# Kernel optimization log

Hardware: AMD Instinct MI355X
Metric: run time of the kernel (lower is better)

Reference implementation:

```python
import jax, jax.numpy as jnp
import numpy as np
import math

B_GRAPHS = 256
L_NODES = 64
N_NODES = B_GRAPHS * L_NODES
N_EDGES = N_NODES * 4
HEADS = 8
D_INNER = 512
N_DAGS = 1
DIAMETER = 64


def setup_inputs() -> dict:
    key = jax.random.key(0)
    ks = jax.random.split(key, 8)
    x = jax.random.normal(ks[0], (N_NODES, D_INNER), jnp.float32)
    B = jax.random.normal(ks[1], (N_NODES, D_INNER), jnp.float32)
    C = jax.random.normal(ks[2], (N_NODES, D_INNER), jnp.float32)
    dt = jax.random.normal(ks[3], (N_NODES, N_DAGS * HEADS * 2), jnp.float32)
    dt_edge = jax.random.normal(ks[4], (N_EDGES, N_DAGS * HEADS), jnp.float32)
    # DAG edges: within each graph, src_local < dst_local (gap 1..7) -> strictly upper triangular
    u = jax.random.randint(ks[5], (N_EDGES,), 0, L_NODES - 1)
    gap = jax.random.randint(ks[6], (N_EDGES,), 1, 8)
    v = jnp.minimum(u + gap, L_NODES - 1)
    graph = jnp.arange(N_EDGES) // (N_EDGES // B_GRAPHS)
    edge_index = jnp.stack([graph * L_NODES + u, graph * L_NODES + v]).astype(jnp.int32)
    data_batch = (jnp.arange(N_NODES) // L_NODES).astype(jnp.int32)
    dag_masks = jnp.ones((N_DAGS, N_EDGES), jnp.float32)
    # dt_bias init as in module __init__ (inverse softplus of dt in [1e-3, 1e-1])
    rng = np.random.default_rng(0)
    dtv = np.exp(rng.uniform(size=(HEADS,)) * (math.log(0.1) - math.log(0.001)) + math.log(0.001))
    dtv = np.clip(dtv, 1e-4, None)
    dt_bias = jnp.asarray(dtv + np.log(-np.expm1(-dtv)), jnp.float32)
    D = jnp.ones((HEADS,), jnp.float32)
    return dict(x=x, B=B, C=C, dt=dt, dt_edge=dt_edge, dt_bias=dt_bias, D=D,
                dag_masks=dag_masks, edge_index=edge_index, data_batch=data_batch,
                diameter=DIAMETER)


def _repeated_squaring_inverse(A, diam):
    # (I - A)^{-1} = prod_k (I + A^{2^k}) for nilpotent A; O(log diam) matmuls
    j = 2 ** int(math.ceil(math.log2(diam)))
    I = jnp.eye(A.shape[-1], dtype=A.dtype)
    last = A
    M = I + A
    for _ in range(2, int(math.log2(j)) + 1):
        last = last @ last
        M = M @ (I + last)
    return M


def reference(x, B, C, dt, dt_edge, dt_bias, D, dag_masks, edge_index, data_batch, diameter):
    N, din = x.shape
    g, E = dag_masks.shape
    n = dt_bias.shape[0]
    b = int(data_batch[-1]) + 1
    l = N // b  # equal-size graphs -> dense batching is a reshape, mask all-True
    h = din // n
    src, dst = edge_index[0], edge_index[1]

    # dt_node: (N, g*n*c) -> (c, g, n, N); softplus(dt + bias)
    c = dt.shape[1] // (g * n)
    dtn = dt.reshape(N, g, n, c).transpose(3, 1, 2, 0)
    dtn = jax.nn.softplus(dtn + dt_bias[None, None, :, None])
    dte = dt_edge.reshape(E, g, n).transpose(1, 2, 0)  # (g,n,E)
    dte = jax.nn.softplus(dte + dt_bias[None, :, None])

    dt_s, dt_t = dtn[0], dtn[1]
    dt_sum = (dt_s[:, :, src] + dt_t[:, :, dst] + dte) / np.sqrt(3.0)  # (g,n,E)
    dt_exp = jnp.exp(-dt_sum)
    msk = dag_masks[:, None, :]
    dt_sum = dt_sum * msk
    dt_exp = dt_exp * msk

    # dense adjacency with per-edge attrs; note 'b l1 l2 (g n) -> b g n l2 l1' transpose
    b_e = src // l
    sl = src % l
    dl = dst % l
    attr = dt_exp.transpose(2, 0, 1).reshape(E, g * n)
    adj = jnp.zeros((b, l, l, g * n), x.dtype).at[b_e, sl, dl].add(attr)
    A = adj.reshape(b, l, l, g, n).transpose(0, 3, 4, 2, 1)  # (b,g,n,l,l)

    # normalize_mat: sqrt outer product of in-degree counts, clamped at 1
    ec = jnp.zeros((g, N), x.dtype).at[:, dst].add(dag_masks)
    ec_dense = ec.T.reshape(b, l, g)
    outer = jnp.sqrt(jnp.einsum('blg,btg->bglt', ec_dense, ec_dense))
    outer = jnp.where(outer < 1.0, 1.0, outer)
    A = A / outer[:, :, None]

    dnorm = jnp.zeros((g, n, N), x.dtype).at[:, :, dst].add(dt_sum)
    dnorm = dnorm.transpose(2, 0, 1).reshape(b, l, g, n).transpose(0, 2, 3, 1)  # (b,g,n,l)

    A2 = A.reshape(b, g * n, l, l).astype(jnp.float32)
    L = _repeated_squaring_inverse(A2, int(diameter))
    L = L.reshape(b, g, n, l, l) * dnorm[..., None]

    x4 = x.reshape(b, l, n, h).transpose(0, 2, 1, 3)  # (b,n,l,h)
    B3 = B.reshape(b, l, -1)
    C3 = C.reshape(b, l, -1)
    # y = einsum(C,L,B,x) with B/C broadcast over (g,n): fold C.B^T into L
    CB = jnp.einsum('bld,btd->blt', C3, B3)
    M = L * CB[:, None, None]
    y = jnp.einsum('bgnlt,bnth->bgnlh', M, x4)
    y = y + x4[:, None] * D[None, None, :, None, None]
    y = y.transpose(0, 3, 1, 2, 4).reshape(N, g, n * h)  # b g n l h -> (N, g, n*h)
    y = y.sum(axis=1) / np.sqrt(g)
    return y
```

## Files before the change

### kernel.cpp

```cpp
#include <hip/hip_runtime.h>
#include <math.h>

#define NGRAPH 256
#define LNODE  64
#define HEADS  8
#define DIN    512
#define EPG    256
#define NEDGE  65536

__device__ __forceinline__ float softplusf(float v) {
    return (v > 20.f) ? v : log1pf(expf(v));
}
__device__ __forceinline__ unsigned short f2bf(float f) {
    union { float f; unsigned u; } c; c.f = f;
    unsigned r = c.u + 0x7fffu + ((c.u >> 16) & 1u);
    return (unsigned short)(r >> 16);
}
__device__ __forceinline__ float bf2f(unsigned short h) {
    union { float f; unsigned u; } c; c.u = ((unsigned)h) << 16;
    return c.f;
}

__global__ __launch_bounds__(256) void cb_kernel(const float* __restrict__ Bm,
                                                 const float* __restrict__ Cm,
                                                 float* __restrict__ CBp,
                                                 int dper, int tposed) {
    int b = blockIdx.x;
    int slice = blockIdx.y;
    __shared__ float Cs[64 * 68];
    __shared__ float Bs[64 * 68];
    int tid = threadIdx.x;
    int ti = tid >> 4, tj = tid & 15;
    float acc[4][4] = {};
    const float* Cg = Cm + (size_t)b * 64 * DIN;
    const float* Bg = Bm + (size_t)b * 64 * DIN;
    int d_lo = slice * dper;
    for (int d0 = d_lo; d0 < d_lo + dper; d0 += 64) {
        __syncthreads();
        #pragma unroll
        for (int k = 0; k < 4; ++k) {
            int f = k * 256 + tid;
            int row = f >> 4;
            int c4 = (f & 15) << 2;
            *(float4*)(Cs + row * 68 + c4) = *(const float4*)(Cg + row * DIN + d0 + c4);
            *(float4*)(Bs + row * 68 + c4) = *(const float4*)(Bg + row * DIN + d0 + c4);
        }
        __syncthreads();
        for (int d = 0; d < 64; d += 4) {
            float4 cr[4], br[4];
            #pragma unroll
            for (int r = 0; r < 4; ++r) cr[r] = *(const float4*)(Cs + (4 * ti + r) * 68 + d);
            #pragma unroll
            for (int c = 0; c < 4; ++c) br[c] = *(const float4*)(Bs + (4 * tj + c) * 68 + d);
            #pragma unroll
            for (int r = 0; r < 4; ++r)
                #pragma unroll
                for (int c = 0; c < 4; ++c)
                    acc[r][c] += cr[r].x * br[c].x + cr[r].y * br[c].y +
                                 cr[r].z * br[c].z + cr[r].w * br[c].w;
        }
    }
    float* outp = CBp + ((size_t)slice * NGRAPH + b) * 4096;
    if (!tposed) {
        #pragma unroll
        for (int r = 0; r < 4; ++r)
            *(float4*)(outp + (4 * ti + r) * 64 + 4 * tj) =
                make_float4(acc[r][0], acc[r][1], acc[r][2], acc[r][3]);
    } else {
        #pragma unroll
        for (int r = 0; r < 4; ++r)
            #pragma unroll
            for (int c = 0; c < 4; ++c)
                outp[(4 * tj + c) * 64 + (4 * ti + r)] = acc[r][c];
    }
}

__global__ __launch_bounds__(256) void prep_kernel(const float* __restrict__ dt,
                                                   const float* __restrict__ dt_edge,
                                                   const float* __restrict__ dt_bias,
                                                   const float* __restrict__ Dp,
                                                   const float* __restrict__ dag_masks,
                                                   const int* __restrict__ edge_index,
                                                   const float* __restrict__ CBp,
                                                   unsigned short* __restrict__ Wtg,
                                                   int nslice) {
    int b = blockIdx.x;
    int hq = blockIdx.y;
    int tid = threadIdx.x;
    int w = tid >> 6;
    int lane = tid & 63;
    int head = hq * 4 + w;

    __shared__ float CBsh[4096];
    __shared__ unsigned short Wt[4][4096];
    __shared__ float Ab[4][512];
    __shared__ float dnsh[4][64];
    __shared__ float dts[4][64];
    __shared__ float dtt[4][64];
    __shared__ float ecsh[4][64];

    for (int s4 = tid; s4 < 1024; s4 += 256) {
        float4 v = make_float4(0.f, 0.f, 0.f, 0.f);
        for (int s = 0; s < nslice; ++s) {
            float4 p = *(const float4*)(CBp + ((size_t)s * NGRAPH + b) * 4096 + s4 * 4);
            v.x += p.x; v.y += p.y; v.z += p.z; v.w += p.w;
        }
        *(float4*)(CBsh + s4 * 4) = v;
    }
    #pragma unroll
    for (int k = 0; k < 8; ++k) Ab[w][k * 64 + lane] = 0.f;
    dnsh[w][lane] = 0.f;
    ecsh[w][lane] = 0.f;
    float bias = dt_bias[head];
    {
        int node = b * 64 + lane;
        dts[w][lane] = softplusf(dt[node * 16 + head * 2 + 0] + bias);
        dtt[w][lane] = softplusf(dt[node * 16 + head * 2 + 1] + bias);
    }
    __syncthreads();

    #pragma unroll
    for (int k = 0; k < 4; ++k) {
        int e = b * EPG + k * 64 + lane;
        int sl = edge_index[e] & 63;
        int dl = edge_index[NEDGE + e] & 63;
        float m = dag_masks[e];
        float de = softplusf(dt_edge[e * HEADS + head] + bias);
        float dsum = (dts[w][sl] + dtt[w][dl] + de) * 0.57735026918962576451f;
        float dexp = expf(-dsum);
        atomicAdd(&Ab[w][dl * 8 + (dl - sl)], dexp * m);
        atomicAdd(&dnsh[w][dl], dsum * m);
        atomicAdd(&ecsh[w][dl], m);
    }

    {
        float eci = ecsh[w][lane];
        #pragma unroll
        for (int d = 1; d < 8; ++d) {
            int s_ = lane - d;
            if (s_ >= 0) {
                float den = sqrtf(eci * ecsh[w][s_]);
                if (den < 1.f) den = 1.f;
                Ab[w][lane * 8 + d] = Ab[w][lane * 8 + d] / den;
            }
        }
    }

    {
        int j = lane;
        float Dh = Dp[head];
        float mwin[7] = {0.f, 0.f, 0.f, 0.f, 0.f, 0.f, 0.f};
        for (int i8 = 0; i8 < 8; ++i8) {
            unsigned pk[4];
            #pragma unroll
            for (int u = 0; u < 8; ++u) {
                int i = i8 * 8 + u;
                float mi = (j == i) ? 1.f : 0.f;
                #pragma unroll
                for (int s = 0; s < 7; ++s) mi += Ab[w][i * 8 + s + 1] * mwin[s];
                float wv = mi * CBsh[i * 64 + j] * dnsh[w][i];
                if (j == i) wv += Dh;
                #pragma unroll
                for (int s = 6; s > 0; --s) mwin[s] = mwin[s - 1];
                mwin[0] = mi;
                unsigned short hb = f2bf(wv);
                if (u & 1) pk[u >> 1] |= ((unsigned)hb) << 16;
                else       pk[u >> 1] = (unsigned)hb;
            }
            int cblk = i8 ^ (j & 7);
            *(uint4*)(&Wt[w][j * 64 + cblk * 8]) = make_uint4(pk[0], pk[1], pk[2], pk[3]);
        }
    }
    __syncthreads();

    {
        size_t ghbase = ((size_t)b * HEADS + head) * 4096;
        int r_off = lane >> 3;
        int ibk = lane & 7;
        #pragma unroll
        for (int r0 = 0; r0 < 64; r0 += 8) {
            int r = r0 + r_off;
            int cblk = ibk ^ (r & 7);
            uint4 v = *(const uint4*)(&Wt[w][r * 64 + cblk * 8]);
            *(uint4*)(Wtg + ghbase + (size_t)r * 64 + ibk * 8) = v;
        }
    }
}

__global__ __launch_bounds__(256) void gemm_kernel(const float* __restrict__ x,
                                                   const unsigned short* __restrict__ Wtg,
                                                   float* __restrict__ out) {
    int b = blockIdx.x;
    int head = blockIdx.y;
    __shared__ unsigned short Wt[64 * 72];
    __shared__ float Xs[64 * 64];
    int tid = threadIdx.x;

    const uint4* wg = (const uint4*)(Wtg + ((size_t)b * HEADS + head) * 4096);
    #pragma unroll
    for (int q = 0; q < 2; ++q) {
        int s = q * 256 + tid;
        int row = s >> 3;
        int c8 = (s & 7) * 8;
        *(uint4*)(&Wt[row * 72 + c8]) = wg[s];
    }
    const float* xg0 = x + (size_t)b * 64 * DIN + head * 64;
    #pragma unroll
    for (int k = 0; k < 4; ++k) {
        int s = k * 256 + tid;
        int row = s >> 4;
        int c4 = (s & 15) << 2;
        *(float4*)(Xs + row * 64 + c4) = *(const float4*)(xg0 + (size_t)row * DIN + c4);
    }
    __syncthreads();

    int ti = tid >> 4, tj = tid & 15;
    float acc[4][4] = {};
    #pragma unroll 4
    for (int t = 0; t < 64; ++t) {
        uint2 wp = *(const uint2*)(&Wt[t * 72 + 4 * ti]);
        float w0 = bf2f((unsigned short)(wp.x & 0xffffu));
        float w1 = bf2f((unsigned short)(wp.x >> 16));
        float w2 = bf2f((unsigned short)(wp.y & 0xffffu));
        float w3 = bf2f((unsigned short)(wp.y >> 16));
        float4 xv = *(const float4*)(Xs + t * 64 + 4 * tj);
        acc[0][0] += w0 * xv.x; acc[0][1] += w0 * xv.y; acc[0][2] += w0 * xv.z; acc[0][3] += w0 * xv.w;
        acc[1][0] += w1 * xv.x; acc[1][1] += w1 * xv.y; acc[1][2] += w1 * xv.z; acc[1][3] += w1 * xv.w;
        acc[2][0] += w2 * xv.x; acc[2][1] += w2 * xv.y; acc[2][2] += w2 * xv.z; acc[2][3] += w2 * xv.w;
        acc[3][0] += w3 * xv.x; acc[3][1] += w3 * xv.y; acc[3][2] += w3 * xv.z; acc[3][3] += w3 * xv.w;
    }
    #pragma unroll
    for (int r = 0; r < 4; ++r) {
        int i = 4 * ti + r;
        *(float4*)(out + ((size_t)(b * 64 + i)) * DIN + head * 64 + 4 * tj) =
            make_float4(acc[r][0], acc[r][1], acc[r][2], acc[r][3]);
    }
}

__global__ __launch_bounds__(256, 4) void fused_kernel(const float* __restrict__ x,
                                                       const float* __restrict__ dt,
                                                       const float* __restrict__ dt_edge,
                                                       const float* __restrict__ dt_bias,
                                                       const float* __restrict__ Dp,
                                                       const float* __restrict__ dag_masks,
                                                       const int* __restrict__ edge_index,
                                                       const float* __restrict__ CBt,
                                                       float* __restrict__ out,
                                                       int nslice) {
    int b = blockIdx.x;
    int head = blockIdx.y;
    __shared__ float Ab[64 * 8];
    __shared__ float Mt[64 * 68];
    __shared__ float Xs[64 * 64];
    __shared__ float dnsh[64];
    __shared__ float ecsh[64];
    __shared__ float dts[64];
    __shared__ float dtt[64];
    int tid = threadIdx.x;

    int t4 = tid >> 2;
    int ib = (tid & 3) << 4;
    float4 cbsum[4];
    #pragma unroll
    for (int g = 0; g < 4; ++g) cbsum[g] = make_float4(0.f, 0.f, 0.f, 0.f);
    for (int s = 0; s < nslice; ++s) {
        const float* p = CBt + ((size_t)s * NGRAPH + b) * 4096 + t4 * 64 + ib;
        #pragma unroll
        for (int g = 0; g < 4; ++g) {
            float4 v = *(const float4*)(p + 4 * g);
            cbsum[g].x += v.x; cbsum[g].y += v.y; cbsum[g].z += v.z; cbsum[g].w += v.w;
        }
    }
    const float* xg0 = x + ((size_t)b * 64) * DIN + head * 64;
    #pragma unroll
    for (int k = 0; k < 4; ++k) {
        int s = k * 256 + tid;
        int row = s >> 4;
        int c4 = (s & 15) << 2;
        *(float4*)(Xs + row * 64 + c4) = *(const float4*)(xg0 + (size_t)row * DIN + c4);
    }
    for (int k = tid; k < 512; k += 256) Ab[k] = 0.f;
    float bias = dt_bias[head];
    if (tid < 64) {
        dnsh[tid] = 0.f;
        ecsh[tid] = 0.f;
        int node = b * 64 + tid;
        dts[tid] = softplusf(dt[node * 16 + head * 2 + 0] + bias);
        dtt[tid] = softplusf(dt[node * 16 + head * 2 + 1] + bias);
    }
    __syncthreads();
    {
        int e = b * EPG + tid;
        int sl = edge_index[e] & 63;
        int dl = edge_index[NEDGE + e] & 63;
        float m = dag_masks[e];
        float de = softplusf(dt_edge[e * HEADS + head] + bias);
        float dsum = (dts[sl] + dtt[dl] + de) * 0.57735026918962576451f;
        float dexp = expf(-dsum);
        atomicAdd(&Ab[dl * 8 + (dl - sl)], dexp * m);
        atomicAdd(&dnsh[dl], dsum * m);
        atomicAdd(&ecsh[dl], m);
    }
    __syncthreads();
    for (int k = tid; k < 512; k += 256) {
        int i = k >> 3, d = k & 7;
        int src = i - d;
        if (d >= 1 && src >= 0) {
            float den = sqrtf(ecsh[i] * ecsh[src]);
            if (den < 1.f) den = 1.f;
            Ab[k] = Ab[k] / den;
        }
    }
    __syncthreads();
    if (tid < 64) {
        int j = tid;
        float mwin[7] = {0.f, 0.f, 0.f, 0.f, 0.f, 0.f, 0.f};
        for (int i = 0; i < 64; ++i) {
            float mi = (j == i) ? 1.f : 0.f;
            #pragma unroll
            for (int s = 0; s < 7; ++s) mi += Ab[i * 8 + s + 1] * mwin[s];
            Mt[j * 65 + i] = mi;
            #pragma unroll
            for (int s = 6; s > 0; --s) mwin[s] = mwin[s - 1];
            mwin[0] = mi;
        }
    }
    __syncthreads();
    {
        float wv[16];
        #pragma unroll
        for (int g = 0; g < 4; ++g) {
            float4 dn4 = *(const float4*)(dnsh + ib + 4 * g);
            wv[4 * g + 0] = Mt[t4 * 65 + ib + 4 * g + 0] * cbsum[g].x * dn4.x;
            wv[4 * g + 1] = Mt[t4 * 65 + ib + 4 * g + 1] * cbsum[g].y * dn4.y;
            wv[4 * g + 2] = Mt[t4 * 65 + ib + 4 * g + 2] * cbsum[g].z * dn4.z;
            wv[4 * g + 3] = Mt[t4 * 65 + ib + 4 * g + 3] * cbsum[g].w * dn4.w;
        }
        __syncthreads();
        #pragma unroll
        for (int g = 0; g < 4; ++g)
            *(float4*)(Mt + t4 * 68 + ib + 4 * g) =
                make_float4(wv[4 * g + 0], wv[4 * g + 1], wv[4 * g + 2], wv[4 * g + 3]);
    }
    __syncthreads();
    int ti = tid >> 4, tj = tid & 15;
    float acc[4][4] = {};
    #pragma unroll 4
    for (int t = 0; t < 64; ++t) {
        float4 w4 = *(const float4*)(Mt + t * 68 + 4 * ti);
        float4 xv = *(const float4*)(Xs + t * 64 + 4 * tj);
        acc[0][0] += w4.x * xv.x; acc[0][1] += w4.x * xv.y; acc[0][2] += w4.x * xv.z; acc[0][3] += w4.x * xv.w;
        acc[1][0] += w4.y * xv.x; acc[1][1] += w4.y * xv.y; acc[1][2] += w4.y * xv.z; acc[1][3] += w4.y * xv.w;
        acc[2][0] += w4.z * xv.x; acc[2][1] += w4.z * xv.y; acc[2][2] += w4.z * xv.z; acc[2][3] += w4.z * xv.w;
        acc[3][0] += w4.w * xv.x; acc[3][1] += w4.w * xv.y; acc[3][2] += w4.w * xv.z; acc[3][3] += w4.w * xv.w;
    }
    float Dh = Dp[head];
    #pragma unroll
    for (int r = 0; r < 4; ++r) {
        int i = 4 * ti + r;
        float4 xres = *(const float4*)(Xs + i * 64 + 4 * tj);
        float4 v;
        v.x = acc[r][0] + xres.x * Dh;
        v.y = acc[r][1] + xres.y * Dh;
        v.z = acc[r][2] + xres.z * Dh;
        v.w = acc[r][3] + xres.w * Dh;
        *(float4*)(out + ((size_t)(b * 64 + i)) * DIN + head * 64 + 4 * tj) = v;
    }
}

extern "C" void kernel_launch(void* const* d_in, const int* in_sizes, int n_in,
                              void* d_out, int out_size, void* d_ws, size_t ws_size,
                              hipStream_t stream) {
    const float* x        = (const float*)d_in[0];
    const float* Bm       = (const float*)d_in[1];
    const float* Cm       = (const float*)d_in[2];
    const float* dt       = (const float*)d_in[3];
    const float* dt_edge  = (const float*)d_in[4];
    const float* dt_bias  = (const float*)d_in[5];
    const float* Dp       = (const float*)d_in[6];
    const float* dag_mask = (const float*)d_in[7];
    const int*   edge_idx = (const int*)d_in[8];
    float* out = (float*)d_out;

    const size_t CBSLICE = (size_t)NGRAPH * 4096 * 4;
    const size_t WBYTES  = (size_t)NGRAPH * HEADS * 4096 * 2;

    int nslice;
    bool fused;
    if (ws_size >= WBYTES + 4 * CBSLICE)      { fused = false; nslice = 4; }
    else if (ws_size >= WBYTES + 2 * CBSLICE) { fused = false; nslice = 2; }
    else if (ws_size >= WBYTES + 1 * CBSLICE) { fused = false; nslice = 1; }
    else { fused = true; nslice = (ws_size >= 4 * CBSLICE) ? 4 : 1; }

    float* CBp = (float*)d_ws;
    int dper = DIN / nslice;

    if (!fused) {
        unsigned short* Wtg = (unsigned short*)((char*)d_ws + nslice * CBSLICE);
        cb_kernel<<<dim3(NGRAPH, nslice), 256, 0, stream>>>(Bm, Cm, CBp, dper, 0);
        prep_kernel<<<dim3(NGRAPH, 2), 256, 0, stream>>>(dt, dt_edge, dt_bias, Dp,
                                                         dag_mask, edge_idx, CBp, Wtg, nslice);
        gemm_kernel<<<dim3(NGRAPH, HEADS), 256, 0, stream>>>(x, Wtg, out);
    } else {
        cb_kernel<<<dim3(NGRAPH, nslice), 256, 0, stream>>>(Bm, Cm, CBp, dper, 1);
        fused_kernel<<<dim3(NGRAPH, HEADS), 256, 0, stream>>>(x, dt, dt_edge, dt_bias, Dp,
                                                              dag_mask, edge_idx, CBp, out, nslice);
    }
}
```

Baseline: 193.3 us.

## Fuse prep and GEMM into one kernel using bf16 MFMA

Result: no change. 192.7 us (-0.3%).

```diff
diff --git a/kernel.cpp b/kernel.cpp
--- a/kernel.cpp
+++ b/kernel.cpp
@@ -7,6 +7,9 @@
 #define DIN    512
 #define EPG    256
 #define NEDGE  65536
+
+typedef short bf16x8 __attribute__((ext_vector_type(8)));
+typedef float f32x4 __attribute__((ext_vector_type(4)));
 
 __device__ __forceinline__ float softplusf(float v) {
     return (v > 20.f) ? v : log1pf(expf(v));
@@ -75,29 +78,29 @@
     }
 }
 
-__global__ __launch_bounds__(256) void prep_kernel(const float* __restrict__ dt,
-                                                   const float* __restrict__ dt_edge,
-                                                   const float* __restrict__ dt_bias,
-                                                   const float* __restrict__ Dp,
-                                                   const float* __restrict__ dag_masks,
-                                                   const int* __restrict__ edge_index,
-                                                   const float* __restrict__ CBp,
-                                                   unsigned short* __restrict__ Wtg,
-                                                   int nslice) {
+__global__ __launch_bounds__(256, 4) void fused2_kernel(const float* __restrict__ x,
+                                                        const float* __restrict__ dt,
+                                                        const float* __restrict__ dt_edge,
+                                                        const float* __restrict__ dt_bias,
+                                                        const float* __restrict__ Dp,
+                                                        const float* __restrict__ dag_masks,
+                                                        const int* __restrict__ edge_index,
+                                                        const float* __restrict__ CBp,
+                                                        float* __restrict__ out,
+                                                        int nslice) {
     int b = blockIdx.x;
-    int hq = blockIdx.y;
+    int head = blockIdx.y;
+    __shared__ unsigned short CBsh[64 * 64];
+    __shared__ unsigned short Wl[64 * 72];
+    __shared__ unsigned short Xt[64 * 72];
+    __shared__ float Ab[512];
+    __shared__ float dnsh[64];
+    __shared__ float ecsh[64];
+    __shared__ float dts[64];
+    __shared__ float dtt[64];
     int tid = threadIdx.x;
     int w = tid >> 6;
     int lane = tid & 63;
-    int head = hq * 4 + w;
-
-    __shared__ float CBsh[4096];
-    __shared__ unsigned short Wt[4][4096];
-    __shared__ float Ab[4][512];
-    __shared__ float dnsh[4][64];
-    __shared__ float dts[4][64];
-    __shared__ float dtt[4][64];
-    __shared__ float ecsh[4][64];
 
     for (int s4 = tid; s4 < 1024; s4 += 256) {
         float4 v = make_float4(0.f, 0.f, 0.f, 0.f);
@@ -105,135 +108,94 @@
             float4 p = *(const float4*)(CBp + ((size_t)s * NGRAPH + b) * 4096 + s4 * 4);
             v.x += p.x; v.y += p.y; v.z += p.z; v.w += p.w;
         }
-        *(float4*)(CBsh + s4 * 4) = v;
-    }
-    #pragma unroll
-    for (int k = 0; k < 8; ++k) Ab[w][k * 64 + lane] = 0.f;
-    dnsh[w][lane] = 0.f;
-    ecsh[w][lane] = 0.f;
-    float bias = dt_bias[head];
-    {
-        int node = b * 64 + lane;
-        dts[w][lane] = softplusf(dt[node * 16 + head * 2 + 0] + bias);
-        dtt[w][lane] = softplusf(dt[node * 16 + head * 2 + 1] + bias);
-    }
-    __syncthreads();
-
-    #pragma unroll
-    for (int k = 0; k < 4; ++k) {
-        int e = b * EPG + k * 64 + lane;
-        int sl = edge_index[e] & 63;
-        int dl = edge_index[NEDGE + e] & 63;
-        float m = dag_masks[e];
-        float de = softplusf(dt_edge[e * HEADS + head] + bias);
-        float dsum = (dts[w][sl] + dtt[w][dl] + de) * 0.57735026918962576451f;
-        float dexp = expf(-dsum);
-        atomicAdd(&Ab[w][dl * 8 + (dl - sl)], dexp * m);
-        atomicAdd(&dnsh[w][dl], dsum * m);
-        atomicAdd(&ecsh[w][dl], m);
-    }
-
-    {
-        float eci = ecsh[w][lane];
-        #pragma unroll
-        for (int d = 1; d < 8; ++d) {
-            int s_ = lane - d;
-            if (s_ >= 0) {
-                float den = sqrtf(eci * ecsh[w][s_]);
-                if (den < 1.f) den = 1.f;
-                Ab[w][lane * 8 + d] = Ab[w][lane * 8 + d] / den;
-            }
-        }
-    }
-
-    {
-        int j = lane;
-        float Dh = Dp[head];
-        float mwin[7] = {0.f, 0.f, 0.f, 0.f, 0.f, 0.f, 0.f};
-        for (int i8 = 0; i8 < 8; ++i8) {
-            unsigned pk[4];
-            #pragma unroll
-            for (int u = 0; u < 8; ++u) {
-                int i = i8 * 8 + u;
-                float mi = (j == i) ? 1.f : 0.f;
-                #pragma unroll
-                for (int s = 0; s < 7; ++s) mi += Ab[w][i * 8 + s + 1] * mwin[s];
-                float wv = mi * CBsh[i * 64 + j] * dnsh[w][i];
-                if (j == i) wv += Dh;
-                #pragma unroll
-                for (int s = 6; s > 0; --s) mwin[s] = mwin[s - 1];
-                mwin[0] = mi;
-                unsigned short hb = f2bf(wv);
-                if (u & 1) pk[u >> 1] |= ((unsigned)hb) << 16;
-                else       pk[u >> 1] = (unsigned)hb;
-            }
-            int cblk = i8 ^ (j & 7);
-            *(uint4*)(&Wt[w][j * 64 + cblk * 8]) = make_uint4(pk[0], pk[1], pk[2], pk[3]);
-        }
-    }
-    __syncthreads();
-
-    {
-        size_t ghbase = ((size_t)b * HEADS + head) * 4096;
-        int r_off = lane >> 3;
-        int ibk = lane & 7;
-        #pragma unroll
-        for (int r0 = 0; r0 < 64; r0 += 8) {
-            int r = r0 + r_off;
-            int cblk = ibk ^ (r & 7);
-            uint4 v = *(const uint4*)(&Wt[w][r * 64 + cblk * 8]);
-            *(uint4*)(Wtg + ghbase + (size_t)r * 64 + ibk * 8) = v;
-        }
-    }
-}
-
-__global__ __launch_bounds__(256) void gemm_kernel(const float* __restrict__ x,
-                                                   const unsigned short* __restrict__ Wtg,
-                                                   float* __restrict__ out) {
-    int b = blockIdx.x;
-    int head = blockIdx.y;
-    __shared__ unsigned short Wt[64 * 72];
-    __shared__ float Xs[64 * 64];
-    int tid = threadIdx.x;
-
-    const uint4* wg = (const uint4*)(Wtg + ((size_t)b * HEADS + head) * 4096);
-    #pragma unroll
-    for (int q = 0; q < 2; ++q) {
-        int s = q * 256 + tid;
-        int row = s >> 3;
-        int c8 = (s & 7) * 8;
-        *(uint4*)(&Wt[row * 72 + c8]) = wg[s];
+        unsigned short* q = &CBsh[s4 * 4];
+        q[0] = f2bf(v.x); q[1] = f2bf(v.y); q[2] = f2bf(v.z); q[3] = f2bf(v.w);
     }
     const float* xg0 = x + (size_t)b * 64 * DIN + head * 64;
     #pragma unroll
     for (int k = 0; k < 4; ++k) {
         int s = k * 256 + tid;
-        int row = s >> 4;
-        int c4 = (s & 15) << 2;
-        *(float4*)(Xs + row * 64 + c4) = *(const float4*)(xg0 + (size_t)row * DIN + c4);
-    }
-    __syncthreads();
-
-    int ti = tid >> 4, tj = tid & 15;
-    float acc[4][4] = {};
-    #pragma unroll 4
-    for (int t = 0; t < 64; ++t) {
-        uint2 wp = *(const uint2*)(&Wt[t * 72 + 4 * ti]);
-        float w0 = bf2f((unsigned short)(wp.x & 0xffffu));
-        float w1 = bf2f((unsigned short)(wp.x >> 16));
-        float w2 = bf2f((unsigned short)(wp.y & 0xffffu));
-        float w3 = bf2f((unsigned short)(wp.y >> 16));
-        float4 xv = *(const float4*)(Xs + t * 64 + 4 * tj);
-        acc[0][0] += w0 * xv.x; acc[0][1] += w0 * xv.y; acc[0][2] += w0 * xv.z; acc[0][3] += w0 * xv.w;
-        acc[1][0] += w1 * xv.x; acc[1][1] += w1 * xv.y; acc[1][2] += w1 * xv.z; acc[1][3] += w1 * xv.w;
-        acc[2][0] += w2 * xv.x; acc[2][1] += w2 * xv.y; acc[2][2] += w2 * xv.z; acc[2][3] += w2 * xv.w;
-        acc[3][0] += w3 * xv.x; acc[3][1] += w3 * xv.y; acc[3][2] += w3 * xv.z; acc[3][3] += w3 * xv.w;
-    }
-    #pragma unroll
-    for (int r = 0; r < 4; ++r) {
-        int i = 4 * ti + r;
-        *(float4*)(out + ((size_t)(b * 64 + i)) * DIN + head * 64 + 4 * tj) =
-            make_float4(acc[r][0], acc[r][1], acc[r][2], acc[r][3]);
+        int t = s >> 4;
+        int e0 = (s & 15) << 2;
+        float4 v = *(const float4*)(xg0 + (size_t)t * DIN + e0);
+        Xt[(e0 + 0) * 72 + t] = f2bf(v.x);
+        Xt[(e0 + 1) * 72 + t] = f2bf(v.y);
+        Xt[(e0 + 2) * 72 + t] = f2bf(v.z);
+        Xt[(e0 + 3) * 72 + t] = f2bf(v.w);
+    }
+    for (int k = tid; k < 512; k += 256) Ab[k] = 0.f;
+    float bias = dt_bias[head];
+    if (tid < 64) {
+        dnsh[tid] = 0.f;
+        ecsh[tid] = 0.f;
+        int node = b * 64 + tid;
+        dts[tid] = softplusf(dt[node * 16 + head * 2 + 0] + bias);
+        dtt[tid] = softplusf(dt[node * 16 + head * 2 + 1] + bias);
+    }
+    __syncthreads();
+
+    {
+        int e = b * EPG + tid;
+        int sl = edge_index[e] & 63;
+        int dl = edge_index[NEDGE + e] & 63;
+        float mk = dag_masks[e];
+        float de = softplusf(dt_edge[e * HEADS + head] + bias);
+        float dsum = (dts[sl] + dtt[dl] + de) * 0.57735026918962576451f;
+        float dexp = expf(-dsum);
+        atomicAdd(&Ab[dl * 8 + (dl - sl)], dexp * mk);
+        atomicAdd(&dnsh[dl], dsum * mk);
+        atomicAdd(&ecsh[dl], mk);
+    }
+    __syncthreads();
+
+    for (int k = tid; k < 512; k += 256) {
+        int i = k >> 3, d = k & 7;
+        int src = i - d;
+        if (d >= 1 && src >= 0) {
+            float den = sqrtf(ecsh[i] * ecsh[src]);
+            if (den < 1.f) den = 1.f;
+            Ab[k] = Ab[k] / den;
+        }
+    }
+    __syncthreads();
+
+    if (w == 0) {
+        int j = lane;
+        float Dh = Dp[head];
+        float mwin[7] = {0.f, 0.f, 0.f, 0.f, 0.f, 0.f, 0.f};
+        for (int i = 0; i < 64; ++i) {
+            float mi = (j == i) ? 1.f : 0.f;
+            #pragma unroll
+            for (int s = 0; s < 7; ++s) mi += Ab[i * 8 + s + 1] * mwin[s];
+            float wv = mi * bf2f(CBsh[i * 64 + j]) * dnsh[i];
+            if (j == i) wv += Dh;
+            Wl[i * 72 + j] = f2bf(wv);
+            #pragma unroll
+            for (int s = 6; s > 0; --s) mwin[s] = mwin[s - 1];
+            mwin[0] = mi;
+        }
+    }
+    __syncthreads();
+
+    {
+        int m = lane & 15;
+        int quad = lane >> 4;
+        bf16x8 a0 = *(const bf16x8*)(&Wl[(16 * w + m) * 72 + quad * 8]);
+        bf16x8 a1 = *(const bf16x8*)(&Wl[(16 * w + m) * 72 + 32 + quad * 8]);
+        float* og = out + ((size_t)b * 64) * DIN + head * 64;
+        #pragma unroll
+        for (int eb = 0; eb < 4; ++eb) {
+            bf16x8 b0 = *(const bf16x8*)(&Xt[(eb * 16 + m) * 72 + quad * 8]);
+            bf16x8 b1 = *(const bf16x8*)(&Xt[(eb * 16 + m) * 72 + 32 + quad * 8]);
+            f32x4 acc = {0.f, 0.f, 0.f, 0.f};
+            acc = __builtin_amdgcn_mfma_f32_16x16x32_bf16(a0, b0, acc, 0, 0, 0);
+            acc = __builtin_amdgcn_mfma_f32_16x16x32_bf16(a1, b1, acc, 0, 0, 0);
+            #pragma unroll
+            for (int r = 0; r < 4; ++r) {
+                int row = 16 * w + quad * 4 + r;
+                og[(size_t)row * DIN + eb * 16 + m] = acc[r];
+            }
+        }
     }
 }
 
@@ -293,13 +255,13 @@
         int e = b * EPG + tid;
         int sl = edge_index[e] & 63;
         int dl = edge_index[NEDGE + e] & 63;
-        float m = dag_masks[e];
+        float mk = dag_masks[e];
         float de = softplusf(dt_edge[e * HEADS + head] + bias);
         float dsum = (dts[sl] + dtt[dl] + de) * 0.57735026918962576451f;
         float dexp = expf(-dsum);
-        atomicAdd(&Ab[dl * 8 + (dl - sl)], dexp * m);
-        atomicAdd(&dnsh[dl], dsum * m);
-        atomicAdd(&ecsh[dl], m);
+        atomicAdd(&Ab[dl * 8 + (dl - sl)], dexp * mk);
+        atomicAdd(&dnsh[dl], dsum * mk);
+        atomicAdd(&ecsh[dl], mk);
     }
     __syncthreads();
     for (int k = tid; k < 512; k += 256) {
@@ -383,26 +345,16 @@
     float* out = (float*)d_out;
 
     const size_t CBSLICE = (size_t)NGRAPH * 4096 * 4;
-    const size_t WBYTES  = (size_t)NGRAPH * HEADS * 4096 * 2;
-
-    int nslice;
-    bool fused;
-    if (ws_size >= WBYTES + 4 * CBSLICE)      { fused = false; nslice = 4; }
-    else if (ws_size >= WBYTES + 2 * CBSLICE) { fused = false; nslice = 2; }
-    else if (ws_size >= WBYTES + 1 * CBSLICE) { fused = false; nslice = 1; }
-    else { fused = true; nslice = (ws_size >= 4 * CBSLICE) ? 4 : 1; }
-
     float* CBp = (float*)d_ws;
-    int dper = DIN / nslice;
-
-    if (!fused) {
-        unsigned short* Wtg = (unsigned short*)((char*)d_ws + nslice * CBSLICE);
-        cb_kernel<<<dim3(NGRAPH, nslice), 256, 0, stream>>>(Bm, Cm, CBp, dper, 0);
-        prep_kernel<<<dim3(NGRAPH, 2), 256, 0, stream>>>(dt, dt_edge, dt_bias, Dp,
-                                                         dag_mask, edge_idx, CBp, Wtg, nslice);
-        gemm_kernel<<<dim3(NGRAPH, HEADS), 256, 0, stream>>>(x, Wtg, out);
+
+    if (ws_size >= 2 * CBSLICE) {
+        int nslice = 2;
+        cb_kernel<<<dim3(NGRAPH, nslice), 256, 0, stream>>>(Bm, Cm, CBp, DIN / nslice, 0);
+        fused2_kernel<<<dim3(NGRAPH, HEADS), 256, 0, stream>>>(x, dt, dt_edge, dt_bias, Dp,
+                                                               dag_mask, edge_idx, CBp, out, nslice);
     } else {
-        cb_kernel<<<dim3(NGRAPH, nslice), 256, 0, stream>>>(Bm, Cm, CBp, dper, 1);
+        int nslice = 1;
+        cb_kernel<<<dim3(NGRAPH, nslice), 256, 0, stream>>>(Bm, Cm, CBp, DIN / nslice, 1);
         fused_kernel<<<dim3(NGRAPH, HEADS), 256, 0, stream>>>(x, dt, dt_edge, dt_bias, Dp,
                                                               dag_mask, edge_idx, CBp, out, nslice);
     }
```
